# Optimization experiments

Hardware: AMD Instinct MI355X
Metric: run time of the kernel (lower is better)

## Reference

```python
import jax, jax.numpy as jnp
import numpy as np

NLAYERS = 4
HEADS = 4
HEAD_DIM = 64
C = HEADS * HEAD_DIM  # 256
MAX_LEN = 1024


def setup_inputs() -> dict:
    key = jax.random.key(0)
    k1, k2, k3 = jax.random.split(key, 3)
    B, S = 16, 1024
    x = jax.random.normal(k1, (B, C, 1, S), dtype=jnp.float32)
    # length is only used via its static shape[0]; values are irrelevant
    length = jnp.zeros((MAX_LEN,), dtype=jnp.int32)
    # per-layer 1x1 conv weights, std=0.1 as in the torch init (squeeze the 1x1 spatial dims)
    w = jax.random.normal(k2, (NLAYERS, C, C), dtype=jnp.float32) * 0.1
    # persistent kv buffer
    kv = jax.random.normal(k3, (NLAYERS, HEADS, MAX_LEN, HEAD_DIM), dtype=jnp.float32) * 0.1
    return {"x": x, "length": length, "w": w, "kv": kv}


def reference(x, length, w, kv):
    B, _, _, S = x.shape
    L = length.shape[0]  # static slice length into kv buffer
    scale = 1.0 / jnp.sqrt(jnp.asarray(HEAD_DIM, dtype=x.dtype))
    for i in range(NLAYERS):
        # 1x1 conv == channel projection: (B,C,1,S) -> (B,C,1,S)
        x = jnp.einsum('oc,bchs->bohs', w[i], x)
        # view (B,4,64,S) then permute -> query (B,H,S,D)
        q = x.reshape(B, HEADS, HEAD_DIM, S).transpose(0, 1, 3, 2)
        kvi = kv[i, :, :L]  # (H, L, D); broadcasts over batch like the (1,H,L,D) torch slice
        # scaled dot-product attention with k == v == kvi
        scores = jnp.einsum('bhsd,hld->bhsl', q, kvi) * scale
        attn = jax.nn.softmax(scores, axis=-1)
        o = jnp.einsum('bhsl,hld->bhsd', attn, kvi)  # (B,H,S,D)
        # permute back and merge heads -> (B,256,1,S)
        x = o.transpose(0, 1, 3, 2).reshape(B, C, 1, S)
    return x
```

## Files before the change

### kernel.cpp

```cpp
#include <hip/hip_runtime.h>

#define NL   4
#define NH   4
#define HD   64
#define CD   256
#define SQL  1024
#define BB   16

typedef _Float16 half8 __attribute__((ext_vector_type(8)));
typedef _Float16 half4 __attribute__((ext_vector_type(4)));
typedef _Float16 half2v __attribute__((ext_vector_type(2)));
typedef float    f32x4 __attribute__((ext_vector_type(4)));
typedef float    f32x16 __attribute__((ext_vector_type(16)));
typedef unsigned short u16x8 __attribute__((ext_vector_type(8)));
typedef unsigned int  uint4v __attribute__((ext_vector_type(4)));

static __device__ __forceinline__ float bf2f(unsigned short u) {
    union { unsigned int i; float f; } v; v.i = ((unsigned int)u) << 16; return v.f;
}
static __device__ __forceinline__ unsigned short f2bf(float f) {
    union { float f; unsigned int i; } v; v.f = f;
    unsigned int u = v.i;
    return (unsigned short)((u + 0x7fffu + ((u >> 16) & 1u)) >> 16);
}

static __device__ __forceinline__ int detect_flag(const void* win) {
    const unsigned int* w = (const unsigned int*)win;
    int cnt = 0;
#pragma unroll 1
    for (int i = 0; i < 64; i++) {
        unsigned int lo = w[i] & 0xFFFFu;
        int e = (int)((lo >> 7) & 0xFF);
        cnt += (e >= 96 && e <= 144) ? 1 : 0;
    }
    return cnt >= 48 ? 1 : 0;
}

__global__ __launch_bounds__(256) void prep_all(const void* __restrict__ xin,
                                                const void* __restrict__ win,
                                                const void* __restrict__ kvin,
                                                _Float16* __restrict__ x16,
                                                _Float16* __restrict__ w16,
                                                _Float16* __restrict__ kaF,
                                                _Float16* __restrict__ vtF) {
    __shared__ __align__(16) _Float16 tile[64][72];
    const int bi = blockIdx.x;
    const int t = threadIdx.x;
    const int isbf = detect_flag(win);

    if (bi < 1024) {
        const int st = bi & 15, ct = (bi >> 4) & 3, b = bi >> 6;
        const int r = t >> 2, seg = t & 3;
        const size_t base = ((size_t)(b * CD + ct * 64 + r)) * SQL + st * 64 + seg * 16;
        float v[16];
        if (isbf) {
            const unsigned short* src = (const unsigned short*)xin + base;
            u16x8 u0 = *(const u16x8*)(src);
            u16x8 u1 = *(const u16x8*)(src + 8);
#pragma unroll
            for (int j = 0; j < 8; j++) { v[j] = bf2f(u0[j]); v[8 + j] = bf2f(u1[j]); }
        } else {
            const float* src = (const float*)xin + base;
#pragma unroll
            for (int c = 0; c < 4; c++) {
                f32x4 a = *(const f32x4*)(src + c * 4);
#pragma unroll
                for (int j = 0; j < 4; j++) v[c * 4 + j] = a[j];
            }
        }
#pragma unroll
        for (int j = 0; j < 16; j++) tile[r][seg * 16 + j] = (_Float16)v[j];
        __syncthreads();
        half8 o0, o1;
#pragma unroll
        for (int j = 0; j < 8; j++) { o0[j] = tile[seg * 16 + j][r]; o1[j] = tile[seg * 16 + 8 + j][r]; }
        _Float16* dt = x16 + ((size_t)(b * SQL + st * 64 + r)) * CD + ct * 64 + seg * 16;
        *(half8*)(dt) = o0;
        *(half8*)(dt + 8) = o1;
    } else if (bi < 1280) {
        const int j2 = bi - 1024;
        const int lt = j2 & 15, ih = j2 >> 4;
        const int r = t >> 2, seg = t & 3;
        const size_t base = ((size_t)(ih * SQL + lt * 64 + r)) * HD + seg * 16;
        float v[16];
        if (isbf) {
            const unsigned short* src = (const unsigned short*)kvin + base;
            u16x8 u0 = *(const u16x8*)(src);
            u16x8 u1 = *(const u16x8*)(src + 8);
#pragma unroll
            for (int j = 0; j < 8; j++) { v[j] = bf2f(u0[j]); v[8 + j] = bf2f(u1[j]); }
        } else {
            const float* src = (const float*)kvin + base;
#pragma unroll
            for (int c = 0; c < 4; c++) {
                f32x4 a = *(const f32x4*)(src + c * 4);
#pragma unroll
                for (int j = 0; j < 4; j++) v[c * 4 + j] = a[j];
            }
        }
#pragma unroll
        for (int j = 0; j < 16; j++) tile[r][seg * 16 + j] = (_Float16)v[j];
        __syncthreads();
        const int l = t & 63, hie = l >> 5, lne = l & 31;
        _Float16* kaB = kaF + ((size_t)ih << 16);
        _Float16* vtB = vtF + ((size_t)ih << 16);
#pragma unroll
        for (int it = 0; it < 2; it++) {
            const int c = (t >> 6) + it * 4;
            half8 ok = *(const half8*)(&tile[(c >> 2) * 32 + lne][(c & 3) * 16 + hie * 8]);
            half8 ov;
#pragma unroll
            for (int j = 0; j < 8; j++)
                ov[j] = tile[(c & 3) * 16 + hie * 8 + j][(c >> 2) * 32 + lne];
            *(half8*)(kaB + ((lt * 8 + c) << 9) + l * 8) = ok;
            *(half8*)(vtB + ((lt * 8 + c) << 9) + l * 8) = ov;
        }
    } else {
        const int i = (bi - 1280) * 256 + t;
        const size_t base = (size_t)i * 8;
        half8 h;
        if (isbf) {
            u16x8 u = *(const u16x8*)((const unsigned short*)win + base);
#pragma unroll
            for (int j = 0; j < 8; j++) h[j] = (_Float16)bf2f(u[j]);
        } else {
            const float* p = (const float*)win + base;
            f32x4 a0 = *(const f32x4*)(p);
            f32x4 a1 = *(const f32x4*)(p + 4);
#pragma unroll
            for (int j = 0; j < 4; j++) { h[j] = (_Float16)a0[j]; h[4 + j] = (_Float16)a1[j]; }
        }
        *(half8*)(w16 + base) = h;
    }
}

__global__ __launch_bounds__(256, 2) void layer_fused(const _Float16* __restrict__ xg,
                                                      _Float16* __restrict__ xout,
                                                      const _Float16* __restrict__ w16,
                                                      const _Float16* __restrict__ kaF,
                                                      const _Float16* __restrict__ vtF,
                                                      const void* __restrict__ win,
                                                      void* __restrict__ outp,
                                                      int L) {
    __shared__ __align__(16) _Float16 kvbuf[2][16384];
    const int sb = blockIdx.x;
    const int h  = blockIdx.y;
    const int b  = blockIdx.z;
    const int t  = threadIdx.x;
    const int wv = t >> 6, lane = t & 63, ln = lane & 31, hi = lane >> 5;
    const int s0 = sb * 128 + wv * 32;

    const _Float16* kaB = kaF + ((size_t)(L * NH + h) << 16);
    const _Float16* vtB = vtF + ((size_t)(L * NH + h) << 16);

    auto stage = [&](int lt, int buf, int hf) {
#pragma unroll
        for (int j = 0; j < 4; j++) {
            const int c = wv * 4 + j;
            const _Float16* src = (c < 8)
                ? kaB + (((lt * 8 + c) << 9))
                : vtB + (((lt * 8 + (c - 8)) << 9));
            __builtin_amdgcn_global_load_lds(
                (const __attribute__((address_space(1))) void*)(src + lane * 8),
                (__attribute__((address_space(3))) void*)(&kvbuf[buf][hf * 8192 + c * 512]),
                16, 0, 0);
        }
    };

    stage(0, 0, 0);
    stage(1, 0, 1);

    f32x16 gacc[2];
#pragma unroll
    for (int dblk = 0; dblk < 2; dblk++)
#pragma unroll
        for (int r = 0; r < 16; r++) gacc[dblk][r] = 0.0f;
    const _Float16* wb = w16 + ((size_t)L << 16) + ((size_t)(h * 64) << 8);
#pragma unroll
    for (int kc = 0; kc < 16; kc++) {
        half8 bx = *(const half8*)(xg + ((size_t)((b << 10) + s0 + ln) << 8) + kc * 16 + hi * 8);
#pragma unroll
        for (int dblk = 0; dblk < 2; dblk++) {
            half8 aw = *(const half8*)(wb + ((size_t)(dblk * 32 + ln) << 8) + kc * 16 + hi * 8);
            gacc[dblk] = __builtin_amdgcn_mfma_f32_32x32x16_f16(aw, bx, gacc[dblk], 0, 0, 0);
        }
    }

    const float sc = 0.180336880111120f;
    half8 qb[4];
#pragma unroll
    for (int dblk = 0; dblk < 2; dblk++)
#pragma unroll
        for (int k1 = 0; k1 < 2; k1++) {
            unsigned int u01 = __builtin_bit_cast(unsigned int,
                __builtin_amdgcn_cvt_pkrtz(gacc[dblk][k1 * 8 + 0] * sc, gacc[dblk][k1 * 8 + 1] * sc));
            unsigned int u23 = __builtin_bit_cast(unsigned int,
                __builtin_amdgcn_cvt_pkrtz(gacc[dblk][k1 * 8 + 2] * sc, gacc[dblk][k1 * 8 + 3] * sc));
            unsigned int w01 = __builtin_bit_cast(unsigned int,
                __builtin_amdgcn_cvt_pkrtz(gacc[dblk][k1 * 8 + 4] * sc, gacc[dblk][k1 * 8 + 5] * sc));
            unsigned int w23 = __builtin_bit_cast(unsigned int,
                __builtin_amdgcn_cvt_pkrtz(gacc[dblk][k1 * 8 + 6] * sc, gacc[dblk][k1 * 8 + 7] * sc));
            asm("v_permlane32_swap_b32 %0, %1" : "+v"(u01), "+v"(w01));
            asm("v_permlane32_swap_b32 %0, %1" : "+v"(u23), "+v"(w23));
            uint4v q; q[0] = u01; q[1] = u23; q[2] = w01; q[3] = w23;
            qb[dblk * 2 + k1] = __builtin_bit_cast(half8, q);
        }

    f32x16 oacc[2];
#pragma unroll
    for (int dblk = 0; dblk < 2; dblk++)
#pragma unroll
        for (int r = 0; r < 16; r++) oacc[dblk][r] = 0.0f;
    f32x4 rsum;
#pragma unroll
    for (int r = 0; r < 4; r++) rsum[r] = 0.0f;

    __syncthreads();

#pragma unroll 1
    for (int ltp = 0; ltp < 8; ltp++) {
        const int buf = ltp & 1;
        if (ltp < 7) { stage(2 * ltp + 2, buf ^ 1, 0); stage(2 * ltp + 3, buf ^ 1, 1); }
#pragma unroll
        for (int sub = 0; sub < 2; sub++) {
            const _Float16* base = &kvbuf[buf][sub * 8192];
            half8 kab[8];
#pragma unroll
            for (int c = 0; c < 8; c++)
                kab[c] = *(const half8*)(base + c * 512 + lane * 8);

            f32x16 stt[2];
#pragma unroll
            for (int lblk = 0; lblk < 2; lblk++)
#pragma unroll
                for (int r = 0; r < 16; r++) stt[lblk][r] = 0.0f;
            __builtin_amdgcn_s_setprio(1);
#pragma unroll
            for (int lblk = 0; lblk < 2; lblk++)
#pragma unroll
                for (int kd = 0; kd < 4; kd++)
                    stt[lblk] = __builtin_amdgcn_mfma_f32_32x32x16_f16(
                        kab[lblk * 4 + kd], qb[kd], stt[lblk], 0, 0, 0);
            __builtin_amdgcn_s_setprio(0);

            half8 vab[8];
#pragma unroll
            for (int c = 0; c < 8; c++)
                vab[c] = *(const half8*)(base + (8 + c) * 512 + lane * 8);

            half8 pb[4];
#pragma unroll
            for (int lblk = 0; lblk < 2; lblk++) {
                float e[16];
#pragma unroll
                for (int r = 0; r < 16; r++) e[r] = __builtin_amdgcn_exp2f(stt[lblk][r]);
#pragma unroll
                for (int g = 0; g < 4; g++)
                    rsum[g] += (e[g * 4 + 0] + e[g * 4 + 1]) + (e[g * 4 + 2] + e[g * 4 + 3]);
#pragma unroll
                for (int k1 = 0; k1 < 2; k1++) {
                    unsigned int u01 = __builtin_bit_cast(unsigned int,
                        __builtin_amdgcn_cvt_pkrtz(e[k1 * 8 + 0], e[k1 * 8 + 1]));
                    unsigned int u23 = __builtin_bit_cast(unsigned int,
                        __builtin_amdgcn_cvt_pkrtz(e[k1 * 8 + 2], e[k1 * 8 + 3]));
                    unsigned int w01 = __builtin_bit_cast(unsigned int,
                        __builtin_amdgcn_cvt_pkrtz(e[k1 * 8 + 4], e[k1 * 8 + 5]));
                    unsigned int w23 = __builtin_bit_cast(unsigned int,
                        __builtin_amdgcn_cvt_pkrtz(e[k1 * 8 + 6], e[k1 * 8 + 7]));
                    asm("v_permlane32_swap_b32 %0, %1" : "+v"(u01), "+v"(w01));
                    asm("v_permlane32_swap_b32 %0, %1" : "+v"(u23), "+v"(w23));
                    uint4v p; p[0] = u01; p[1] = u23; p[2] = w01; p[3] = w23;
                    pb[lblk * 2 + k1] = __builtin_bit_cast(half8, p);
                }
            }

            __builtin_amdgcn_s_setprio(1);
#pragma unroll
            for (int dblk = 0; dblk < 2; dblk++)
#pragma unroll
                for (int ks = 0; ks < 4; ks++)
                    oacc[dblk] = __builtin_amdgcn_mfma_f32_32x32x16_f16(
                        vab[dblk * 4 + ks], pb[ks], oacc[dblk], 0, 0, 0);
            __builtin_amdgcn_s_setprio(0);
        }
        __syncthreads();
    }

    float rs = (rsum[0] + rsum[1]) + (rsum[2] + rsum[3]);
    unsigned int ra = __builtin_bit_cast(unsigned int, rs);
    unsigned int rb = ra;
    asm("" : "+v"(rb));
    asm("v_permlane32_swap_b32 %0, %1" : "+v"(ra), "+v"(rb));
    const float inv = 1.0f / (__builtin_bit_cast(float, ra) + __builtin_bit_cast(float, rb));
    const int s = s0 + ln;

    if (L < NL - 1) {
#pragma unroll
        for (int dblk = 0; dblk < 2; dblk++)
#pragma unroll
            for (int q2 = 0; q2 < 4; q2++) {
                half4 hv;
#pragma unroll
                for (int r = 0; r < 4; r++) hv[r] = (_Float16)(oacc[dblk][q2 * 4 + r] * inv);
                *(half4*)(xout + (((size_t)((b << 10) + s)) << 8) +
                          (h << 6) + dblk * 32 + q2 * 8 + hi * 4) = hv;
            }
    } else if (detect_flag(win)) {
#pragma unroll
        for (int dblk = 0; dblk < 2; dblk++)
#pragma unroll
            for (int q2 = 0; q2 < 4; q2++)
#pragma unroll
                for (int r = 0; r < 4; r++) {
                    const int c = (h << 6) + dblk * 32 + q2 * 8 + hi * 4 + r;
                    ((unsigned short*)outp)[(((size_t)(b * CD + c)) << 10) + s] =
                        f2bf(oacc[dblk][q2 * 4 + r] * inv);
                }
    } else {
#pragma unroll
        for (int dblk = 0; dblk < 2; dblk++)
#pragma unroll
            for (int q2 = 0; q2 < 4; q2++)
#pragma unroll
                for (int r = 0; r < 4; r++) {
                    const int c = (h << 6) + dblk * 32 + q2 * 8 + hi * 4 + r;
                    ((float*)outp)[(((size_t)(b * CD + c)) << 10) + s] =
                        oacc[dblk][q2 * 4 + r] * inv;
                }
    }
}

extern "C" void kernel_launch(void* const* d_in, const int* in_sizes, int n_in,
                              void* d_out, int out_size, void* d_ws, size_t ws_size,
                              hipStream_t stream) {
    const void* xin = d_in[0];
    const void* win = d_in[2];
    const void* kvin = d_in[3];

    char* ws = (char*)d_ws;
    const size_t MB = 1u << 20;
    _Float16* xa  = (_Float16*)(ws);
    _Float16* xb  = (_Float16*)(ws + 8 * MB);
    _Float16* w16 = (_Float16*)(ws + 16 * MB);
    _Float16* kaF = (_Float16*)(ws + 17 * MB);
    _Float16* vtF = (_Float16*)(ws + 19 * MB);

    prep_all<<<dim3(1024 + 256 + 128), 256, 0, stream>>>(xin, win, kvin, xa, w16, kaF, vtF);

    _Float16* cur = xa;
    _Float16* nxt = xb;
    for (int i = 0; i < NL; i++) {
        layer_fused<<<dim3(SQL / 128, NH, BB), 256, 0, stream>>>(cur, nxt, w16, kaF, vtF,
                                                                 win, d_out, i);
        _Float16* tmp = cur; cur = nxt; nxt = tmp;
    }
}
```

Baseline: 204.4 us.

## Software-pipeline two KV sub-tiles per stage and cache dtype flag in workspace

The attention inner loop now processes both KV sub-tiles of a stage interleaved. The QK^T MFMAs of the second half overlap the exp/convert work of the first, and the order of the two halves is staggered by a per-wave parity so that waves hit different LDS regions. The dtype-detection scan is vectorised into 16-byte loads. Its result is computed once in prep and stored to workspace, so the last layer kernel no longer rescans the weights. The interleaving roughly doubles live score and operand registers, which risks spills or lower occupancy under the 2-blocks-per-SM launch bound.

```diff
diff --git a/kernel.cpp b/kernel.cpp
--- a/kernel.cpp
+++ b/kernel.cpp
@@ -25,14 +25,19 @@
 }
 
 static __device__ __forceinline__ int detect_flag(const void* win) {
-    const unsigned int* w = (const unsigned int*)win;
+    const uint4v* w = (const uint4v*)win;
     int cnt = 0;
-#pragma unroll 1
-    for (int i = 0; i < 64; i++) {
-        unsigned int lo = w[i] & 0xFFFFu;
-        int e = (int)((lo >> 7) & 0xFF);
-        cnt += (e >= 96 && e <= 144) ? 1 : 0;
-    }
+    uint4v u[16];
+#pragma unroll
+    for (int i = 0; i < 16; i++) u[i] = w[i];
+#pragma unroll
+    for (int i = 0; i < 16; i++)
+#pragma unroll
+        for (int j = 0; j < 4; j++) {
+            unsigned int lo = u[i][j] & 0xFFFFu;
+            int e = (int)((lo >> 7) & 0xFF);
+            cnt += (e >= 96 && e <= 144) ? 1 : 0;
+        }
     return cnt >= 48 ? 1 : 0;
 }
 
@@ -42,7 +47,8 @@
                                                 _Float16* __restrict__ x16,
                                                 _Float16* __restrict__ w16,
                                                 _Float16* __restrict__ kaF,
-                                                _Float16* __restrict__ vtF) {
+                                                _Float16* __restrict__ vtF,
+                                                int* __restrict__ flagp) {
     __shared__ __align__(16) _Float16 tile[64][72];
     const int bi = blockIdx.x;
     const int t = threadIdx.x;
@@ -116,6 +122,7 @@
             *(half8*)(vtB + ((lt * 8 + c) << 9) + l * 8) = ov;
         }
     } else {
+        if (bi == 1280 && t == 0) *flagp = isbf;
         const int i = (bi - 1280) * 256 + t;
         const size_t base = (size_t)i * 8;
         half8 h;
@@ -139,7 +146,7 @@
                                                       const _Float16* __restrict__ w16,
                                                       const _Float16* __restrict__ kaF,
                                                       const _Float16* __restrict__ vtF,
-                                                      const void* __restrict__ win,
+                                                      const int* __restrict__ flagp,
                                                       void* __restrict__ outp,
                                                       int L) {
     __shared__ __align__(16) _Float16 kvbuf[2][16384];
@@ -149,6 +156,9 @@
     const int t  = threadIdx.x;
     const int wv = t >> 6, lane = t & 63, ln = lane & 31, hi = lane >> 5;
     const int s0 = sb * 128 + wv * 32;
+    const int par = (sb ^ h ^ b ^ wv) & 1;
+
+    const int isbf_final = (L == NL - 1) ? *flagp : 0;
 
     const _Float16* kaB = kaF + ((size_t)(L * NH + h) << 16);
     const _Float16* vtB = vtF + ((size_t)(L * NH + h) << 16);
@@ -221,68 +231,118 @@
     for (int ltp = 0; ltp < 8; ltp++) {
         const int buf = ltp & 1;
         if (ltp < 7) { stage(2 * ltp + 2, buf ^ 1, 0); stage(2 * ltp + 3, buf ^ 1, 1); }
-#pragma unroll
-        for (int sub = 0; sub < 2; sub++) {
-            const _Float16* base = &kvbuf[buf][sub * 8192];
-            half8 kab[8];
-#pragma unroll
-            for (int c = 0; c < 8; c++)
-                kab[c] = *(const half8*)(base + c * 512 + lane * 8);
-
-            f32x16 stt[2];
-#pragma unroll
-            for (int lblk = 0; lblk < 2; lblk++)
-#pragma unroll
-                for (int r = 0; r < 16; r++) stt[lblk][r] = 0.0f;
-            __builtin_amdgcn_s_setprio(1);
-#pragma unroll
-            for (int lblk = 0; lblk < 2; lblk++)
-#pragma unroll
-                for (int kd = 0; kd < 4; kd++)
-                    stt[lblk] = __builtin_amdgcn_mfma_f32_32x32x16_f16(
-                        kab[lblk * 4 + kd], qb[kd], stt[lblk], 0, 0, 0);
-            __builtin_amdgcn_s_setprio(0);
-
-            half8 vab[8];
-#pragma unroll
-            for (int c = 0; c < 8; c++)
-                vab[c] = *(const half8*)(base + (8 + c) * 512 + lane * 8);
-
-            half8 pb[4];
-#pragma unroll
-            for (int lblk = 0; lblk < 2; lblk++) {
-                float e[16];
-#pragma unroll
-                for (int r = 0; r < 16; r++) e[r] = __builtin_amdgcn_exp2f(stt[lblk][r]);
-#pragma unroll
-                for (int g = 0; g < 4; g++)
-                    rsum[g] += (e[g * 4 + 0] + e[g * 4 + 1]) + (e[g * 4 + 2] + e[g * 4 + 3]);
-#pragma unroll
-                for (int k1 = 0; k1 < 2; k1++) {
-                    unsigned int u01 = __builtin_bit_cast(unsigned int,
-                        __builtin_amdgcn_cvt_pkrtz(e[k1 * 8 + 0], e[k1 * 8 + 1]));
-                    unsigned int u23 = __builtin_bit_cast(unsigned int,
-                        __builtin_amdgcn_cvt_pkrtz(e[k1 * 8 + 2], e[k1 * 8 + 3]));
-                    unsigned int w01 = __builtin_bit_cast(unsigned int,
-                        __builtin_amdgcn_cvt_pkrtz(e[k1 * 8 + 4], e[k1 * 8 + 5]));
-                    unsigned int w23 = __builtin_bit_cast(unsigned int,
-                        __builtin_amdgcn_cvt_pkrtz(e[k1 * 8 + 6], e[k1 * 8 + 7]));
-                    asm("v_permlane32_swap_b32 %0, %1" : "+v"(u01), "+v"(w01));
-                    asm("v_permlane32_swap_b32 %0, %1" : "+v"(u23), "+v"(w23));
-                    uint4v p; p[0] = u01; p[1] = u23; p[2] = w01; p[3] = w23;
-                    pb[lblk * 2 + k1] = __builtin_bit_cast(half8, p);
-                }
+
+        const _Float16* baseA = &kvbuf[buf][par * 8192];
+        const _Float16* baseB = &kvbuf[buf][(par ^ 1) * 8192];
+
+        half8 kabA[8], kabB[8];
+#pragma unroll
+        for (int c = 0; c < 8; c++) kabA[c] = *(const half8*)(baseA + c * 512 + lane * 8);
+#pragma unroll
+        for (int c = 0; c < 8; c++) kabB[c] = *(const half8*)(baseB + c * 512 + lane * 8);
+
+        f32x16 sttA[2], sttB[2];
+#pragma unroll
+        for (int lblk = 0; lblk < 2; lblk++)
+#pragma unroll
+            for (int r = 0; r < 16; r++) { sttA[lblk][r] = 0.0f; sttB[lblk][r] = 0.0f; }
+
+        __builtin_amdgcn_s_setprio(1);
+#pragma unroll
+        for (int lblk = 0; lblk < 2; lblk++)
+#pragma unroll
+            for (int kd = 0; kd < 4; kd++)
+                sttA[lblk] = __builtin_amdgcn_mfma_f32_32x32x16_f16(
+                    kabA[lblk * 4 + kd], qb[kd], sttA[lblk], 0, 0, 0);
+        __builtin_amdgcn_s_setprio(0);
+
+        half8 vabA[8];
+#pragma unroll
+        for (int c = 0; c < 8; c++) vabA[c] = *(const half8*)(baseA + (8 + c) * 512 + lane * 8);
+
+        __builtin_amdgcn_s_setprio(1);
+#pragma unroll
+        for (int lblk = 0; lblk < 2; lblk++)
+#pragma unroll
+            for (int kd = 0; kd < 4; kd++)
+                sttB[lblk] = __builtin_amdgcn_mfma_f32_32x32x16_f16(
+                    kabB[lblk * 4 + kd], qb[kd], sttB[lblk], 0, 0, 0);
+        __builtin_amdgcn_s_setprio(0);
+
+        half8 pbA[4];
+#pragma unroll
+        for (int lblk = 0; lblk < 2; lblk++) {
+            float e[16];
+#pragma unroll
+            for (int r = 0; r < 16; r++) e[r] = __builtin_amdgcn_exp2f(sttA[lblk][r]);
+#pragma unroll
+            for (int g = 0; g < 4; g++)
+                rsum[g] += (e[g * 4 + 0] + e[g * 4 + 1]) + (e[g * 4 + 2] + e[g * 4 + 3]);
+#pragma unroll
+            for (int k1 = 0; k1 < 2; k1++) {
+                unsigned int u01 = __builtin_bit_cast(unsigned int,
+                    __builtin_amdgcn_cvt_pkrtz(e[k1 * 8 + 0], e[k1 * 8 + 1]));
+                unsigned int u23 = __builtin_bit_cast(unsigned int,
+                    __builtin_amdgcn_cvt_pkrtz(e[k1 * 8 + 2], e[k1 * 8 + 3]));
+                unsigned int w01 = __builtin_bit_cast(unsigned int,
+                    __builtin_amdgcn_cvt_pkrtz(e[k1 * 8 + 4], e[k1 * 8 + 5]));
+                unsigned int w23 = __builtin_bit_cast(unsigned int,
+                    __builtin_amdgcn_cvt_pkrtz(e[k1 * 8 + 6], e[k1 * 8 + 7]));
+                asm("v_permlane32_swap_b32 %0, %1" : "+v"(u01), "+v"(w01));
+                asm("v_permlane32_swap_b32 %0, %1" : "+v"(u23), "+v"(w23));
+                uint4v p; p[0] = u01; p[1] = u23; p[2] = w01; p[3] = w23;
+                pbA[lblk * 2 + k1] = __builtin_bit_cast(half8, p);
             }
-
-            __builtin_amdgcn_s_setprio(1);
-#pragma unroll
-            for (int dblk = 0; dblk < 2; dblk++)
-#pragma unroll
-                for (int ks = 0; ks < 4; ks++)
-                    oacc[dblk] = __builtin_amdgcn_mfma_f32_32x32x16_f16(
-                        vab[dblk * 4 + ks], pb[ks], oacc[dblk], 0, 0, 0);
-            __builtin_amdgcn_s_setprio(0);
-        }
+        }
+
+        half8 vabB[8];
+#pragma unroll
+        for (int c = 0; c < 8; c++) vabB[c] = *(const half8*)(baseB + (8 + c) * 512 + lane * 8);
+
+        __builtin_amdgcn_s_setprio(1);
+#pragma unroll
+        for (int dblk = 0; dblk < 2; dblk++)
+#pragma unroll
+            for (int ks = 0; ks < 4; ks++)
+                oacc[dblk] = __builtin_amdgcn_mfma_f32_32x32x16_f16(
+                    vabA[dblk * 4 + ks], pbA[ks], oacc[dblk], 0, 0, 0);
+        __builtin_amdgcn_s_setprio(0);
+
+        half8 pbB[4];
+#pragma unroll
+        for (int lblk = 0; lblk < 2; lblk++) {
+            float e[16];
+#pragma unroll
+            for (int r = 0; r < 16; r++) e[r] = __builtin_amdgcn_exp2f(sttB[lblk][r]);
+#pragma unroll
+            for (int g = 0; g < 4; g++)
+                rsum[g] += (e[g * 4 + 0] + e[g * 4 + 1]) + (e[g * 4 + 2] + e[g * 4 + 3]);
+#pragma unroll
+            for (int k1 = 0; k1 < 2; k1++) {
+                unsigned int u01 = __builtin_bit_cast(unsigned int,
+                    __builtin_amdgcn_cvt_pkrtz(e[k1 * 8 + 0], e[k1 * 8 + 1]));
+                unsigned int u23 = __builtin_bit_cast(unsigned int,
+                    __builtin_amdgcn_cvt_pkrtz(e[k1 * 8 + 2], e[k1 * 8 + 3]));
+                unsigned int w01 = __builtin_bit_cast(unsigned int,
+                    __builtin_amdgcn_cvt_pkrtz(e[k1 * 8 + 4], e[k1 * 8 + 5]));
+                unsigned int w23 = __builtin_bit_cast(unsigned int,
+                    __builtin_amdgcn_cvt_pkrtz(e[k1 * 8 + 6], e[k1 * 8 + 7]));
+                asm("v_permlane32_swap_b32 %0, %1" : "+v"(u01), "+v"(w01));
+                asm("v_permlane32_swap_b32 %0, %1" : "+v"(u23), "+v"(w23));
+                uint4v p; p[0] = u01; p[1] = u23; p[2] = w01; p[3] = w23;
+                pbB[lblk * 2 + k1] = __builtin_bit_cast(half8, p);
+            }
+        }
+
+        __builtin_amdgcn_s_setprio(1);
+#pragma unroll
+        for (int dblk = 0; dblk < 2; dblk++)
+#pragma unroll
+            for (int ks = 0; ks < 4; ks++)
+                oacc[dblk] = __builtin_amdgcn_mfma_f32_32x32x16_f16(
+                    vabB[dblk * 4 + ks], pbB[ks], oacc[dblk], 0, 0, 0);
+        __builtin_amdgcn_s_setprio(0);
+
         __syncthreads();
     }
 
@@ -305,7 +365,7 @@
                 *(half4*)(xout + (((size_t)((b << 10) + s)) << 8) +
                           (h << 6) + dblk * 32 + q2 * 8 + hi * 4) = hv;
             }
-    } else if (detect_flag(win)) {
+    } else if (isbf_final) {
 #pragma unroll
         for (int dblk = 0; dblk < 2; dblk++)
 #pragma unroll
@@ -344,14 +404,15 @@
     _Float16* w16 = (_Float16*)(ws + 16 * MB);
     _Float16* kaF = (_Float16*)(ws + 17 * MB);
     _Float16* vtF = (_Float16*)(ws + 19 * MB);
-
-    prep_all<<<dim3(1024 + 256 + 128), 256, 0, stream>>>(xin, win, kvin, xa, w16, kaF, vtF);
+    int*      flg = (int*)(ws + 21 * MB);
+
+    prep_all<<<dim3(1024 + 256 + 128), 256, 0, stream>>>(xin, win, kvin, xa, w16, kaF, vtF, flg);
 
     _Float16* cur = xa;
     _Float16* nxt = xb;
     for (int i = 0; i < NL; i++) {
         layer_fused<<<dim3(SQL / 128, NH, BB), 256, 0, stream>>>(cur, nxt, w16, kaF, vtF,
-                                                                 win, d_out, i);
+                                                                 flg, d_out, i);
         _Float16* tmp = cur; cur = nxt; nxt = tmp;
     }
 }
```

Result: no change. 201.4 us (-1.4%).

## Split KV sequence across two wave groups per block with LDS reduction

Applied to the files above, without the earlier changes.

Blocks grow from 256 to 512 threads. Two groups of four waves each process half of the KV length: tiles 0-7 and tiles 8-15. Their partial output accumulators and row sums are combined through LDS at the end. The aim is more waves in flight to hide latency, at the cost of an extra reduction, a sync, and duplicated Q projection work in both halves. The dtype-detection flag is now computed once in the prep kernel and read from workspace, and detect_flag is vectorised.

```diff
diff --git a/kernel.cpp b/kernel.cpp
--- a/kernel.cpp
+++ b/kernel.cpp
@@ -25,14 +25,19 @@
 }
 
 static __device__ __forceinline__ int detect_flag(const void* win) {
-    const unsigned int* w = (const unsigned int*)win;
+    const uint4v* w = (const uint4v*)win;
     int cnt = 0;
-#pragma unroll 1
-    for (int i = 0; i < 64; i++) {
-        unsigned int lo = w[i] & 0xFFFFu;
-        int e = (int)((lo >> 7) & 0xFF);
-        cnt += (e >= 96 && e <= 144) ? 1 : 0;
-    }
+    uint4v u[16];
+#pragma unroll
+    for (int i = 0; i < 16; i++) u[i] = w[i];
+#pragma unroll
+    for (int i = 0; i < 16; i++)
+#pragma unroll
+        for (int j = 0; j < 4; j++) {
+            unsigned int lo = u[i][j] & 0xFFFFu;
+            int e = (int)((lo >> 7) & 0xFF);
+            cnt += (e >= 96 && e <= 144) ? 1 : 0;
+        }
     return cnt >= 48 ? 1 : 0;
 }
 
@@ -42,7 +47,8 @@
                                                 _Float16* __restrict__ x16,
                                                 _Float16* __restrict__ w16,
                                                 _Float16* __restrict__ kaF,
-                                                _Float16* __restrict__ vtF) {
+                                                _Float16* __restrict__ vtF,
+                                                int* __restrict__ flagp) {
     __shared__ __align__(16) _Float16 tile[64][72];
     const int bi = blockIdx.x;
     const int t = threadIdx.x;
@@ -116,6 +122,7 @@
             *(half8*)(vtB + ((lt * 8 + c) << 9) + l * 8) = ov;
         }
     } else {
+        if (bi == 1280 && t == 0) *flagp = isbf;
         const int i = (bi - 1280) * 256 + t;
         const size_t base = (size_t)i * 8;
         half8 h;
@@ -134,41 +141,45 @@
     }
 }
 
-__global__ __launch_bounds__(256, 2) void layer_fused(const _Float16* __restrict__ xg,
+#define STAGE_TILE(kaB_, vtB_, lt_, buf_, hf_)                                         \
+    do {                                                                               \
+        _Pragma("unroll")                                                              \
+        for (int j = 0; j < 2; j++) {                                                  \
+            const int c = wv * 2 + j;                                                  \
+            const _Float16* src = (c < 8)                                              \
+                ? (kaB_) + ((((lt_) * 8 + c) << 9))                                    \
+                : (vtB_) + ((((lt_) * 8 + (c - 8)) << 9));                             \
+            __builtin_amdgcn_global_load_lds(                                          \
+                (const __attribute__((address_space(1))) void*)(src + lane * 8),       \
+                (__attribute__((address_space(3))) void*)(&kvbuf[(buf_)][(hf_)][c * 512]), \
+                16, 0, 0);                                                             \
+        }                                                                              \
+    } while (0)
+
+__global__ __launch_bounds__(512, 4) void layer_fused(const _Float16* __restrict__ xg,
                                                       _Float16* __restrict__ xout,
                                                       const _Float16* __restrict__ w16,
                                                       const _Float16* __restrict__ kaF,
                                                       const _Float16* __restrict__ vtF,
-                                                      const void* __restrict__ win,
+                                                      const int* __restrict__ flagp,
                                                       void* __restrict__ outp,
                                                       int L) {
-    __shared__ __align__(16) _Float16 kvbuf[2][16384];
+    __shared__ __align__(16) _Float16 kvbuf[2][2][8192];
     const int sb = blockIdx.x;
     const int h  = blockIdx.y;
     const int b  = blockIdx.z;
     const int t  = threadIdx.x;
     const int wv = t >> 6, lane = t & 63, ln = lane & 31, hi = lane >> 5;
-    const int s0 = sb * 128 + wv * 32;
+    const int sg = wv & 3, hl = wv >> 2;
+    const int s0 = sb * 128 + sg * 32;
+
+    const int isbf_final = (L == NL - 1) ? *flagp : 0;
 
     const _Float16* kaB = kaF + ((size_t)(L * NH + h) << 16);
     const _Float16* vtB = vtF + ((size_t)(L * NH + h) << 16);
 
-    auto stage = [&](int lt, int buf, int hf) {
-#pragma unroll
-        for (int j = 0; j < 4; j++) {
-            const int c = wv * 4 + j;
-            const _Float16* src = (c < 8)
-                ? kaB + (((lt * 8 + c) << 9))
-                : vtB + (((lt * 8 + (c - 8)) << 9));
-            __builtin_amdgcn_global_load_lds(
-                (const __attribute__((address_space(1))) void*)(src + lane * 8),
-                (__attribute__((address_space(3))) void*)(&kvbuf[buf][hf * 8192 + c * 512]),
-                16, 0, 0);
-        }
-    };
-
-    stage(0, 0, 0);
-    stage(1, 0, 1);
+    STAGE_TILE(kaB, vtB, 0, 0, 0);
+    STAGE_TILE(kaB, vtB, 8, 0, 1);
 
     f32x16 gacc[2];
 #pragma unroll
@@ -220,113 +231,135 @@
 #pragma unroll 1
     for (int ltp = 0; ltp < 8; ltp++) {
         const int buf = ltp & 1;
-        if (ltp < 7) { stage(2 * ltp + 2, buf ^ 1, 0); stage(2 * ltp + 3, buf ^ 1, 1); }
-#pragma unroll
-        for (int sub = 0; sub < 2; sub++) {
-            const _Float16* base = &kvbuf[buf][sub * 8192];
-            half8 kab[8];
-#pragma unroll
-            for (int c = 0; c < 8; c++)
-                kab[c] = *(const half8*)(base + c * 512 + lane * 8);
-
-            f32x16 stt[2];
-#pragma unroll
-            for (int lblk = 0; lblk < 2; lblk++)
-#pragma unroll
-                for (int r = 0; r < 16; r++) stt[lblk][r] = 0.0f;
-            __builtin_amdgcn_s_setprio(1);
-#pragma unroll
-            for (int lblk = 0; lblk < 2; lblk++)
-#pragma unroll
-                for (int kd = 0; kd < 4; kd++)
-                    stt[lblk] = __builtin_amdgcn_mfma_f32_32x32x16_f16(
-                        kab[lblk * 4 + kd], qb[kd], stt[lblk], 0, 0, 0);
-            __builtin_amdgcn_s_setprio(0);
-
-            half8 vab[8];
-#pragma unroll
-            for (int c = 0; c < 8; c++)
-                vab[c] = *(const half8*)(base + (8 + c) * 512 + lane * 8);
-
-            half8 pb[4];
-#pragma unroll
-            for (int lblk = 0; lblk < 2; lblk++) {
-                float e[16];
-#pragma unroll
-                for (int r = 0; r < 16; r++) e[r] = __builtin_amdgcn_exp2f(stt[lblk][r]);
-#pragma unroll
-                for (int g = 0; g < 4; g++)
-                    rsum[g] += (e[g * 4 + 0] + e[g * 4 + 1]) + (e[g * 4 + 2] + e[g * 4 + 3]);
-#pragma unroll
-                for (int k1 = 0; k1 < 2; k1++) {
-                    unsigned int u01 = __builtin_bit_cast(unsigned int,
-                        __builtin_amdgcn_cvt_pkrtz(e[k1 * 8 + 0], e[k1 * 8 + 1]));
-                    unsigned int u23 = __builtin_bit_cast(unsigned int,
-                        __builtin_amdgcn_cvt_pkrtz(e[k1 * 8 + 2], e[k1 * 8 + 3]));
-                    unsigned int w01 = __builtin_bit_cast(unsigned int,
-                        __builtin_amdgcn_cvt_pkrtz(e[k1 * 8 + 4], e[k1 * 8 + 5]));
-                    unsigned int w23 = __builtin_bit_cast(unsigned int,
-                        __builtin_amdgcn_cvt_pkrtz(e[k1 * 8 + 6], e[k1 * 8 + 7]));
-                    asm("v_permlane32_swap_b32 %0, %1" : "+v"(u01), "+v"(w01));
-                    asm("v_permlane32_swap_b32 %0, %1" : "+v"(u23), "+v"(w23));
-                    uint4v p; p[0] = u01; p[1] = u23; p[2] = w01; p[3] = w23;
-                    pb[lblk * 2 + k1] = __builtin_bit_cast(half8, p);
+        if (ltp < 7) {
+            STAGE_TILE(kaB, vtB, ltp + 1, buf ^ 1, 0);
+            STAGE_TILE(kaB, vtB, 9 + ltp, buf ^ 1, 1);
+        }
+
+        const _Float16* base = &kvbuf[buf][hl][0];
+
+        half8 kab[8];
+#pragma unroll
+        for (int c = 0; c < 8; c++) kab[c] = *(const half8*)(base + c * 512 + lane * 8);
+
+        f32x16 stt[2];
+#pragma unroll
+        for (int lblk = 0; lblk < 2; lblk++)
+#pragma unroll
+            for (int r = 0; r < 16; r++) stt[lblk][r] = 0.0f;
+
+        __builtin_amdgcn_s_setprio(1);
+#pragma unroll
+        for (int lblk = 0; lblk < 2; lblk++)
+#pragma unroll
+            for (int kd = 0; kd < 4; kd++)
+                stt[lblk] = __builtin_amdgcn_mfma_f32_32x32x16_f16(
+                    kab[lblk * 4 + kd], qb[kd], stt[lblk], 0, 0, 0);
+        __builtin_amdgcn_s_setprio(0);
+
+        half8 vab[8];
+#pragma unroll
+        for (int c = 0; c < 8; c++) vab[c] = *(const half8*)(base + (8 + c) * 512 + lane * 8);
+
+        half8 pb[4];
+#pragma unroll
+        for (int lblk = 0; lblk < 2; lblk++) {
+            float e[16];
+#pragma unroll
+            for (int r = 0; r < 16; r++) e[r] = __builtin_amdgcn_exp2f(stt[lblk][r]);
+#pragma unroll
+            for (int g = 0; g < 4; g++)
+                rsum[g] += (e[g * 4 + 0] + e[g * 4 + 1]) + (e[g * 4 + 2] + e[g * 4 + 3]);
+#pragma unroll
+            for (int k1 = 0; k1 < 2; k1++) {
+                unsigned int u01 = __builtin_bit_cast(unsigned int,
+                    __builtin_amdgcn_cvt_pkrtz(e[k1 * 8 + 0], e[k1 * 8 + 1]));
+                unsigned int u23 = __builtin_bit_cast(unsigned int,
+                    __builtin_amdgcn_cvt_pkrtz(e[k1 * 8 + 2], e[k1 * 8 + 3]));
+                unsigned int w01 = __builtin_bit_cast(unsigned int,
+                    __builtin_amdgcn_cvt_pkrtz(e[k1 * 8 + 4], e[k1 * 8 + 5]));
+                unsigned int w23 = __builtin_bit_cast(unsigned int,
+                    __builtin_amdgcn_cvt_pkrtz(e[k1 * 8 + 6], e[k1 * 8 + 7]));
+                asm("v_permlane32_swap_b32 %0, %1" : "+v"(u01), "+v"(w01));
+                asm("v_permlane32_swap_b32 %0, %1" : "+v"(u23), "+v"(w23));
+                uint4v p; p[0] = u01; p[1] = u23; p[2] = w01; p[3] = w23;
+                pb[lblk * 2 + k1] = __builtin_bit_cast(half8, p);
+            }
+        }
+
+        __builtin_amdgcn_s_setprio(1);
+#pragma unroll
+        for (int dblk = 0; dblk < 2; dblk++)
+#pragma unroll
+            for (int ks = 0; ks < 4; ks++)
+                oacc[dblk] = __builtin_amdgcn_mfma_f32_32x32x16_f16(
+                    vab[dblk * 4 + ks], pb[ks], oacc[dblk], 0, 0, 0);
+        __builtin_amdgcn_s_setprio(0);
+
+        __syncthreads();
+    }
+
+    float rs = (rsum[0] + rsum[1]) + (rsum[2] + rsum[3]);
+    float* scr = (float*)(&kvbuf[0][0][0]);
+    const int sidx = (sg * 64 + lane) * 37;
+
+    if (hl == 1) {
+#pragma unroll
+        for (int dblk = 0; dblk < 2; dblk++)
+#pragma unroll
+            for (int r = 0; r < 16; r++) scr[sidx + dblk * 16 + r] = oacc[dblk][r];
+        scr[sidx + 32] = rs;
+    }
+    __syncthreads();
+
+    if (hl == 0) {
+#pragma unroll
+        for (int dblk = 0; dblk < 2; dblk++)
+#pragma unroll
+            for (int r = 0; r < 16; r++) oacc[dblk][r] += scr[sidx + dblk * 16 + r];
+        rs += scr[sidx + 32];
+
+        unsigned int ra = __builtin_bit_cast(unsigned int, rs);
+        unsigned int rb = ra;
+        asm("" : "+v"(rb));
+        asm("v_permlane32_swap_b32 %0, %1" : "+v"(ra), "+v"(rb));
+        const float inv = 1.0f / (__builtin_bit_cast(float, ra) + __builtin_bit_cast(float, rb));
+        const int s = s0 + ln;
+
+        if (L < NL - 1) {
+#pragma unroll
+            for (int dblk = 0; dblk < 2; dblk++)
+#pragma unroll
+                for (int q2 = 0; q2 < 4; q2++) {
+                    half4 hv;
+#pragma unroll
+                    for (int r = 0; r < 4; r++) hv[r] = (_Float16)(oacc[dblk][q2 * 4 + r] * inv);
+                    *(half4*)(xout + (((size_t)((b << 10) + s)) << 8) +
+                              (h << 6) + dblk * 32 + q2 * 8 + hi * 4) = hv;
                 }
-            }
-
-            __builtin_amdgcn_s_setprio(1);
+        } else if (isbf_final) {
 #pragma unroll
             for (int dblk = 0; dblk < 2; dblk++)
 #pragma unroll
-                for (int ks = 0; ks < 4; ks++)
-                    oacc[dblk] = __builtin_amdgcn_mfma_f32_32x32x16_f16(
-                        vab[dblk * 4 + ks], pb[ks], oacc[dblk], 0, 0, 0);
-            __builtin_amdgcn_s_setprio(0);
-        }
-        __syncthreads();
-    }
-
-    float rs = (rsum[0] + rsum[1]) + (rsum[2] + rsum[3]);
-    unsigned int ra = __builtin_bit_cast(unsigned int, rs);
-    unsigned int rb = ra;
-    asm("" : "+v"(rb));
-    asm("v_permlane32_swap_b32 %0, %1" : "+v"(ra), "+v"(rb));
-    const float inv = 1.0f / (__builtin_bit_cast(float, ra) + __builtin_bit_cast(float, rb));
-    const int s = s0 + ln;
-
-    if (L < NL - 1) {
-#pragma unroll
-        for (int dblk = 0; dblk < 2; dblk++)
-#pragma unroll
-            for (int q2 = 0; q2 < 4; q2++) {
-                half4 hv;
-#pragma unroll
-                for (int r = 0; r < 4; r++) hv[r] = (_Float16)(oacc[dblk][q2 * 4 + r] * inv);
-                *(half4*)(xout + (((size_t)((b << 10) + s)) << 8) +
-                          (h << 6) + dblk * 32 + q2 * 8 + hi * 4) = hv;
-            }
-    } else if (detect_flag(win)) {
-#pragma unroll
-        for (int dblk = 0; dblk < 2; dblk++)
-#pragma unroll
-            for (int q2 = 0; q2 < 4; q2++)
-#pragma unroll
-                for (int r = 0; r < 4; r++) {
-                    const int c = (h << 6) + dblk * 32 + q2 * 8 + hi * 4 + r;
-                    ((unsigned short*)outp)[(((size_t)(b * CD + c)) << 10) + s] =
-                        f2bf(oacc[dblk][q2 * 4 + r] * inv);
-                }
-    } else {
-#pragma unroll
-        for (int dblk = 0; dblk < 2; dblk++)
-#pragma unroll
-            for (int q2 = 0; q2 < 4; q2++)
-#pragma unroll
-                for (int r = 0; r < 4; r++) {
-                    const int c = (h << 6) + dblk * 32 + q2 * 8 + hi * 4 + r;
-                    ((float*)outp)[(((size_t)(b * CD + c)) << 10) + s] =
-                        oacc[dblk][q2 * 4 + r] * inv;
-                }
+                for (int q2 = 0; q2 < 4; q2++)
+#pragma unroll
+                    for (int r = 0; r < 4; r++) {
+                        const int c = (h << 6) + dblk * 32 + q2 * 8 + hi * 4 + r;
+                        ((unsigned short*)outp)[(((size_t)(b * CD + c)) << 10) + s] =
+                            f2bf(oacc[dblk][q2 * 4 + r] * inv);
+                    }
+        } else {
+#pragma unroll
+            for (int dblk = 0; dblk < 2; dblk++)
+#pragma unroll
+                for (int q2 = 0; q2 < 4; q2++)
+#pragma unroll
+                    for (int r = 0; r < 4; r++) {
+                        const int c = (h << 6) + dblk * 32 + q2 * 8 + hi * 4 + r;
+                        ((float*)outp)[(((size_t)(b * CD + c)) << 10) + s] =
+                            oacc[dblk][q2 * 4 + r] * inv;
+                    }
+        }
     }
 }
 
@@ -344,14 +377,15 @@
     _Float16* w16 = (_Float16*)(ws + 16 * MB);
     _Float16* kaF = (_Float16*)(ws + 17 * MB);
     _Float16* vtF = (_Float16*)(ws + 19 * MB);
-
-    prep_all<<<dim3(1024 + 256 + 128), 256, 0, stream>>>(xin, win, kvin, xa, w16, kaF, vtF);
+    int*      flg = (int*)(ws + 21 * MB);
+
+    prep_all<<<dim3(1024 + 256 + 128), 256, 0, stream>>>(xin, win, kvin, xa, w16, kaF, vtF, flg);
 
     _Float16* cur = xa;
     _Float16* nxt = xb;
     for (int i = 0; i < NL; i++) {
-        layer_fused<<<dim3(SQL / 128, NH, BB), 256, 0, stream>>>(cur, nxt, w16, kaF, vtF,
-                                                                 win, d_out, i);
+        layer_fused<<<dim3(SQL / 128, NH, BB), 512, 0, stream>>>(cur, nxt, w16, kaF, vtF,
+                                                                 flg, d_out, i);
         _Float16* tmp = cur; cur = nxt; nxt = tmp;
     }
 }
```

Measured after the change: 305.0 us. +49.2%, slower.

## Load K/V fragments directly from global into registers instead of LDS staging

Applied to the files above, without the earlier changes.

The attention loop no longer stages K and V tiles into shared memory with global_load_lds and barriers. Each wave now loads its MFMA operand fragments straight from global (L2-resident) memory into registers, double-buffered across tiles, and the launch-bounds occupancy hint is removed. The dtype detection result is computed once in the prep kernel and stored in a workspace flag rather than re-scanned in the last layer, and the scan itself is vectorised. This removes LDS traffic and block-wide syncs but raises register pressure and makes every wave fetch the same K/V data from L2 separately.

```diff
diff --git a/kernel.cpp b/kernel.cpp
--- a/kernel.cpp
+++ b/kernel.cpp
@@ -25,14 +25,19 @@
 }
 
 static __device__ __forceinline__ int detect_flag(const void* win) {
-    const unsigned int* w = (const unsigned int*)win;
+    const uint4v* w = (const uint4v*)win;
     int cnt = 0;
-#pragma unroll 1
-    for (int i = 0; i < 64; i++) {
-        unsigned int lo = w[i] & 0xFFFFu;
-        int e = (int)((lo >> 7) & 0xFF);
-        cnt += (e >= 96 && e <= 144) ? 1 : 0;
-    }
+    uint4v u[16];
+#pragma unroll
+    for (int i = 0; i < 16; i++) u[i] = w[i];
+#pragma unroll
+    for (int i = 0; i < 16; i++)
+#pragma unroll
+        for (int j = 0; j < 4; j++) {
+            unsigned int lo = u[i][j] & 0xFFFFu;
+            int e = (int)((lo >> 7) & 0xFF);
+            cnt += (e >= 96 && e <= 144) ? 1 : 0;
+        }
     return cnt >= 48 ? 1 : 0;
 }
 
@@ -42,7 +47,8 @@
                                                 _Float16* __restrict__ x16,
                                                 _Float16* __restrict__ w16,
                                                 _Float16* __restrict__ kaF,
-                                                _Float16* __restrict__ vtF) {
+                                                _Float16* __restrict__ vtF,
+                                                int* __restrict__ flagp) {
     __shared__ __align__(16) _Float16 tile[64][72];
     const int bi = blockIdx.x;
     const int t = threadIdx.x;
@@ -116,6 +122,7 @@
             *(half8*)(vtB + ((lt * 8 + c) << 9) + l * 8) = ov;
         }
     } else {
+        if (bi == 1280 && t == 0) *flagp = isbf;
         const int i = (bi - 1280) * 256 + t;
         const size_t base = (size_t)i * 8;
         half8 h;
@@ -134,15 +141,14 @@
     }
 }
 
-__global__ __launch_bounds__(256, 2) void layer_fused(const _Float16* __restrict__ xg,
-                                                      _Float16* __restrict__ xout,
-                                                      const _Float16* __restrict__ w16,
-                                                      const _Float16* __restrict__ kaF,
-                                                      const _Float16* __restrict__ vtF,
-                                                      const void* __restrict__ win,
-                                                      void* __restrict__ outp,
-                                                      int L) {
-    __shared__ __align__(16) _Float16 kvbuf[2][16384];
+__global__ __launch_bounds__(256) void layer_fused(const _Float16* __restrict__ xg,
+                                                   _Float16* __restrict__ xout,
+                                                   const _Float16* __restrict__ w16,
+                                                   const _Float16* __restrict__ kaF,
+                                                   const _Float16* __restrict__ vtF,
+                                                   const int* __restrict__ flagp,
+                                                   void* __restrict__ outp,
+                                                   int L) {
     const int sb = blockIdx.x;
     const int h  = blockIdx.y;
     const int b  = blockIdx.z;
@@ -150,25 +156,10 @@
     const int wv = t >> 6, lane = t & 63, ln = lane & 31, hi = lane >> 5;
     const int s0 = sb * 128 + wv * 32;
 
-    const _Float16* kaB = kaF + ((size_t)(L * NH + h) << 16);
-    const _Float16* vtB = vtF + ((size_t)(L * NH + h) << 16);
-
-    auto stage = [&](int lt, int buf, int hf) {
-#pragma unroll
-        for (int j = 0; j < 4; j++) {
-            const int c = wv * 4 + j;
-            const _Float16* src = (c < 8)
-                ? kaB + (((lt * 8 + c) << 9))
-                : vtB + (((lt * 8 + (c - 8)) << 9));
-            __builtin_amdgcn_global_load_lds(
-                (const __attribute__((address_space(1))) void*)(src + lane * 8),
-                (__attribute__((address_space(3))) void*)(&kvbuf[buf][hf * 8192 + c * 512]),
-                16, 0, 0);
-        }
-    };
-
-    stage(0, 0, 0);
-    stage(1, 0, 1);
+    const int isbf_final = (L == NL - 1) ? *flagp : 0;
+
+    const _Float16* kaB = kaF + ((size_t)(L * NH + h) << 16) + lane * 8;
+    const _Float16* vtB = vtF + ((size_t)(L * NH + h) << 16) + lane * 8;
 
     f32x16 gacc[2];
 #pragma unroll
@@ -215,76 +206,85 @@
 #pragma unroll
     for (int r = 0; r < 4; r++) rsum[r] = 0.0f;
 
-    __syncthreads();
+    auto process = [&](const half8* ka, const half8* va) {
+        f32x16 stt[2];
+#pragma unroll
+        for (int lblk = 0; lblk < 2; lblk++)
+#pragma unroll
+            for (int r = 0; r < 16; r++) stt[lblk][r] = 0.0f;
+        __builtin_amdgcn_s_setprio(1);
+#pragma unroll
+        for (int lblk = 0; lblk < 2; lblk++)
+#pragma unroll
+            for (int kd = 0; kd < 4; kd++)
+                stt[lblk] = __builtin_amdgcn_mfma_f32_32x32x16_f16(
+                    ka[lblk * 4 + kd], qb[kd], stt[lblk], 0, 0, 0);
+        __builtin_amdgcn_s_setprio(0);
+
+        half8 pb[4];
+#pragma unroll
+        for (int lblk = 0; lblk < 2; lblk++) {
+            float e[16];
+#pragma unroll
+            for (int r = 0; r < 16; r++) e[r] = __builtin_amdgcn_exp2f(stt[lblk][r]);
+#pragma unroll
+            for (int g = 0; g < 4; g++)
+                rsum[g] += (e[g * 4 + 0] + e[g * 4 + 1]) + (e[g * 4 + 2] + e[g * 4 + 3]);
+#pragma unroll
+            for (int k1 = 0; k1 < 2; k1++) {
+                unsigned int u01 = __builtin_bit_cast(unsigned int,
+                    __builtin_amdgcn_cvt_pkrtz(e[k1 * 8 + 0], e[k1 * 8 + 1]));
+                unsigned int u23 = __builtin_bit_cast(unsigned int,
+                    __builtin_amdgcn_cvt_pkrtz(e[k1 * 8 + 2], e[k1 * 8 + 3]));
+                unsigned int w01 = __builtin_bit_cast(unsigned int,
+                    __builtin_amdgcn_cvt_pkrtz(e[k1 * 8 + 4], e[k1 * 8 + 5]));
+                unsigned int w23 = __builtin_bit_cast(unsigned int,
+                    __builtin_amdgcn_cvt_pkrtz(e[k1 * 8 + 6], e[k1 * 8 + 7]));
+                asm("v_permlane32_swap_b32 %0, %1" : "+v"(u01), "+v"(w01));
+                asm("v_permlane32_swap_b32 %0, %1" : "+v"(u23), "+v"(w23));
+                uint4v p; p[0] = u01; p[1] = u23; p[2] = w01; p[3] = w23;
+                pb[lblk * 2 + k1] = __builtin_bit_cast(half8, p);
+            }
+        }
+
+        __builtin_amdgcn_s_setprio(1);
+#pragma unroll
+        for (int dblk = 0; dblk < 2; dblk++)
+#pragma unroll
+            for (int ks = 0; ks < 4; ks++)
+                oacc[dblk] = __builtin_amdgcn_mfma_f32_32x32x16_f16(
+                    va[dblk * 4 + ks], pb[ks], oacc[dblk], 0, 0, 0);
+        __builtin_amdgcn_s_setprio(0);
+    };
+
+#define LOADK(dst, lt)                                                        \
+    do {                                                                      \
+        _Pragma("unroll")                                                     \
+        for (int c = 0; c < 8; c++)                                           \
+            dst[c] = *(const half8*)(kaB + (((lt) * 8 + c) << 9));            \
+    } while (0)
+#define LOADV(dst, lt)                                                        \
+    do {                                                                      \
+        _Pragma("unroll")                                                     \
+        for (int c = 0; c < 8; c++)                                           \
+            dst[c] = *(const half8*)(vtB + (((lt) * 8 + c) << 9));            \
+    } while (0)
+
+    half8 ka0[8], ka1[8], va[8];
+    LOADK(ka0, 0);
+    LOADV(va, 0);
 
 #pragma unroll 1
-    for (int ltp = 0; ltp < 8; ltp++) {
-        const int buf = ltp & 1;
-        if (ltp < 7) { stage(2 * ltp + 2, buf ^ 1, 0); stage(2 * ltp + 3, buf ^ 1, 1); }
-#pragma unroll
-        for (int sub = 0; sub < 2; sub++) {
-            const _Float16* base = &kvbuf[buf][sub * 8192];
-            half8 kab[8];
-#pragma unroll
-            for (int c = 0; c < 8; c++)
-                kab[c] = *(const half8*)(base + c * 512 + lane * 8);
-
-            f32x16 stt[2];
-#pragma unroll
-            for (int lblk = 0; lblk < 2; lblk++)
-#pragma unroll
-                for (int r = 0; r < 16; r++) stt[lblk][r] = 0.0f;
-            __builtin_amdgcn_s_setprio(1);
-#pragma unroll
-            for (int lblk = 0; lblk < 2; lblk++)
-#pragma unroll
-                for (int kd = 0; kd < 4; kd++)
-                    stt[lblk] = __builtin_amdgcn_mfma_f32_32x32x16_f16(
-                        kab[lblk * 4 + kd], qb[kd], stt[lblk], 0, 0, 0);
-            __builtin_amdgcn_s_setprio(0);
-
-            half8 vab[8];
-#pragma unroll
-            for (int c = 0; c < 8; c++)
-                vab[c] = *(const half8*)(base + (8 + c) * 512 + lane * 8);
-
-            half8 pb[4];
-#pragma unroll
-            for (int lblk = 0; lblk < 2; lblk++) {
-                float e[16];
-#pragma unroll
-                for (int r = 0; r < 16; r++) e[r] = __builtin_amdgcn_exp2f(stt[lblk][r]);
-#pragma unroll
-                for (int g = 0; g < 4; g++)
-                    rsum[g] += (e[g * 4 + 0] + e[g * 4 + 1]) + (e[g * 4 + 2] + e[g * 4 + 3]);
-#pragma unroll
-                for (int k1 = 0; k1 < 2; k1++) {
-                    unsigned int u01 = __builtin_bit_cast(unsigned int,
-                        __builtin_amdgcn_cvt_pkrtz(e[k1 * 8 + 0], e[k1 * 8 + 1]));
-                    unsigned int u23 = __builtin_bit_cast(unsigned int,
-                        __builtin_amdgcn_cvt_pkrtz(e[k1 * 8 + 2], e[k1 * 8 + 3]));
-                    unsigned int w01 = __builtin_bit_cast(unsigned int,
-                        __builtin_amdgcn_cvt_pkrtz(e[k1 * 8 + 4], e[k1 * 8 + 5]));
-                    unsigned int w23 = __builtin_bit_cast(unsigned int,
-                        __builtin_amdgcn_cvt_pkrtz(e[k1 * 8 + 6], e[k1 * 8 + 7]));
-                    asm("v_permlane32_swap_b32 %0, %1" : "+v"(u01), "+v"(w01));
-                    asm("v_permlane32_swap_b32 %0, %1" : "+v"(u23), "+v"(w23));
-                    uint4v p; p[0] = u01; p[1] = u23; p[2] = w01; p[3] = w23;
-                    pb[lblk * 2 + k1] = __builtin_bit_cast(half8, p);
-                }
-            }
-
-            __builtin_amdgcn_s_setprio(1);
-#pragma unroll
-            for (int dblk = 0; dblk < 2; dblk++)
-#pragma unroll
-                for (int ks = 0; ks < 4; ks++)
-                    oacc[dblk] = __builtin_amdgcn_mfma_f32_32x32x16_f16(
-                        vab[dblk * 4 + ks], pb[ks], oacc[dblk], 0, 0, 0);
-            __builtin_amdgcn_s_setprio(0);
-        }
-        __syncthreads();
-    }
+    for (int lt = 0; lt < 16; lt += 2) {
+        LOADK(ka1, lt + 1);
+        process(ka0, va);
+        LOADV(va, lt + 1);
+        if (lt + 2 < 16) LOADK(ka0, lt + 2);
+        process(ka1, va);
+        if (lt + 2 < 16) LOADV(va, lt + 2);
+    }
+#undef LOADK
+#undef LOADV
 
     float rs = (rsum[0] + rsum[1]) + (rsum[2] + rsum[3]);
     unsigned int ra = __builtin_bit_cast(unsigned int, rs);
@@ -305,7 +305,7 @@
                 *(half4*)(xout + (((size_t)((b << 10) + s)) << 8) +
                           (h << 6) + dblk * 32 + q2 * 8 + hi * 4) = hv;
             }
-    } else if (detect_flag(win)) {
+    } else if (isbf_final) {
 #pragma unroll
         for (int dblk = 0; dblk < 2; dblk++)
 #pragma unroll
@@ -344,14 +344,15 @@
     _Float16* w16 = (_Float16*)(ws + 16 * MB);
     _Float16* kaF = (_Float16*)(ws + 17 * MB);
     _Float16* vtF = (_Float16*)(ws + 19 * MB);
-
-    prep_all<<<dim3(1024 + 256 + 128), 256, 0, stream>>>(xin, win, kvin, xa, w16, kaF, vtF);
+    int*      flg = (int*)(ws + 21 * MB);
+
+    prep_all<<<dim3(1024 + 256 + 128), 256, 0, stream>>>(xin, win, kvin, xa, w16, kaF, vtF, flg);
 
     _Float16* cur = xa;
     _Float16* nxt = xb;
     for (int i = 0; i < NL; i++) {
         layer_fused<<<dim3(SQL / 128, NH, BB), 256, 0, stream>>>(cur, nxt, w16, kaF, vtF,
-                                                                 win, d_out, i);
+                                                                 flg, d_out, i);
         _Float16* tmp = cur; cur = nxt; nxt = tmp;
     }
 }
```

New measurement: 216.1 us. 5.7% more time.
